# Optimization experiments

Hardware: AMD Instinct MI355X
Metric: run time of the kernel (lower is better)

Reference implementation:

```python
import jax, jax.numpy as jnp
import numpy as np

B, S, D = 4, 4096, 768  # batch, seq_len, n_units
NEG = -1000000000.0      # masked_fill value from the torch source


def setup_inputs() -> dict:
    key = jax.random.key(0)
    ks = jax.random.split(key, 12)
    scale = 1.0 / np.sqrt(D)
    inp = {
        "query": jax.random.normal(ks[0], (B, S, D), jnp.float32),
        "key_": jax.random.normal(ks[1], (B, S, D), jnp.float32),
        "value": jax.random.normal(ks[2], (B, S, D), jnp.float32),
        # nn.Linear weights are [out, in]; forward computes x @ W.T + b
        "Wq": jax.random.normal(ks[3], (D, D), jnp.float32) * scale,
        "bq": jnp.zeros((D,), jnp.float32),
        "Wk": jax.random.normal(ks[4], (D, D), jnp.float32) * scale,
        "bk": jnp.zeros((D,), jnp.float32),
        "Wv": jax.random.normal(ks[5], (D, D), jnp.float32) * scale,
        "bv": jnp.zeros((D,), jnp.float32),
        "Wo": jax.random.normal(ks[6], (D, D), jnp.float32) * scale,
        "bo": jnp.zeros((D,), jnp.float32),
        # broadcastable causal mask [1, S, S]; 0 -> masked
        "mask": jnp.tril(jnp.ones((S, S), jnp.int32))[None, :, :],
    }
    return inp


def reference(query, key_, value, Wq, bq, Wk, bk, Wv, bv, Wo, bo, mask):
    # QKV projections (torch Linear: x @ W.T + b)
    q = jnp.einsum("bsd,ed->bse", query, Wq) + bq
    k = jnp.einsum("bsd,ed->bse", key_, Wk) + bk
    v = jnp.einsum("bsd,ed->bse", value, Wv) + bv
    # scores: NOTE source scales by n_units**0.5 (full model dim, no head split)
    weights = jnp.einsum("bqd,bkd->bqk", q, k) / jnp.sqrt(jnp.float32(D))
    weights = jnp.where(mask == 0, jnp.float32(NEG), weights)
    weights = jax.nn.softmax(weights, axis=-1)
    # dropout is identity in eval/deterministic reference
    attended = jnp.einsum("bqk,bkd->bqd", weights, v)
    return jnp.einsum("bsd,ed->bse", attended, Wo) + bo
```

## Files before the change

kernel.cpp:

```cpp
#include <hip/hip_runtime.h>
#include <hip/hip_bf16.h>
#include <stdint.h>

#define DI __device__ __forceinline__

typedef __bf16 bf16x4 __attribute__((ext_vector_type(4)));
typedef __bf16 bf16x8 __attribute__((ext_vector_type(8)));
typedef float  f32x4  __attribute__((ext_vector_type(4)));

static constexpr int  BATCH = 4;
static constexpr int  SEQ   = 4096;
static constexpr int  DIM   = 768;
static constexpr long TOK   = (long)BATCH * SEQ;
static constexpr int  QT    = SEQ / 128;
static constexpr int  NTRI  = QT * (QT + 1) / 2;
static constexpr float SCALE = 0.0360843918243516150f;

__global__ void cvt3_kernel(const float* __restrict__ a, const float* __restrict__ b,
                            const float* __restrict__ c, __bf16* __restrict__ oa,
                            __bf16* __restrict__ ob, __bf16* __restrict__ oc, long n4){
  const float* in  = blockIdx.y == 0 ? a : blockIdx.y == 1 ? b : c;
  __bf16*      out = blockIdx.y == 0 ? oa : blockIdx.y == 1 ? ob : oc;
  long i = (long)blockIdx.x * blockDim.x + threadIdx.x;
  const long stride = (long)gridDim.x * blockDim.x;
  for(; i < n4; i += stride){
    float4 v = ((const float4*)in)[i];
    bf16x4 o = { (__bf16)v.x, (__bf16)v.y, (__bf16)v.z, (__bf16)v.w };
    ((bf16x4*)out)[i] = o;
  }
}
__global__ void cvt4_kernel(const float* __restrict__ a, const float* __restrict__ b,
                            const float* __restrict__ c, const float* __restrict__ d,
                            __bf16* __restrict__ oa, __bf16* __restrict__ ob,
                            __bf16* __restrict__ oc, __bf16* __restrict__ od, long n4){
  const float* in  = blockIdx.y == 0 ? a : blockIdx.y == 1 ? b : blockIdx.y == 2 ? c : d;
  __bf16*      out = blockIdx.y == 0 ? oa : blockIdx.y == 1 ? ob : blockIdx.y == 2 ? oc : od;
  long i = (long)blockIdx.x * blockDim.x + threadIdx.x;
  const long stride = (long)gridDim.x * blockDim.x;
  for(; i < n4; i += stride){
    float4 v = ((const float4*)in)[i];
    bf16x4 o = { (__bf16)v.x, (__bf16)v.y, (__bf16)v.z, (__bf16)v.w };
    ((bf16x4*)out)[i] = o;
  }
}

DI int swz_off(int r, int c){ return (r << 7) + ((c ^ (r & 7)) << 4); }

template<int R>
DI void stage(const __bf16* __restrict__ src, long ld, char* lds, int tid){
  const int w = tid >> 6, l = tid & 63;
  const int rsub = l >> 3;
  const int kc   = (l & 7) ^ rsub;
  const __bf16* g = src + (long)(w * 8 + rsub) * ld + kc * 8;
  char* d = lds + (w << 10);
  #pragma unroll
  for(int i = 0; i < R / 64; ++i){
    __builtin_amdgcn_global_load_lds(
        (const __attribute__((address_space(1))) void*)(g + (long)(i * 64) * ld),
        (__attribute__((address_space(3))) void*)(d + i * 8192), 16, 0, 0);
  }
}

DI bf16x8 frag_ld(const char* lds, int row, int c){
  return *(const bf16x8*)(lds + swz_off(row, c));
}

DI void mma_tile(const char* As, const char* Bs, int lane, int wr, int wc, f32x4 acc[4][4]){
  #pragma unroll
  for(int kk = 0; kk < 2; ++kk){
    const int c = kk * 4 + (lane >> 4);
    bf16x8 a[4], b[4];
    #pragma unroll
    for(int i = 0; i < 4; ++i) a[i] = frag_ld(As, wr + i * 16 + (lane & 15), c);
    #pragma unroll
    for(int j = 0; j < 4; ++j) b[j] = frag_ld(Bs, wc + j * 16 + (lane & 15), c);
    #pragma unroll
    for(int i = 0; i < 4; ++i)
      #pragma unroll
      for(int j = 0; j < 4; ++j)
        acc[i][j] = __builtin_amdgcn_mfma_f32_16x16x32_bf16(a[i], b[j], acc[i][j], 0, 0, 0);
  }
}

template<class FA, class FB>
DI void kloop2(FA fa, long lda, FB fb, long ldb, int nt, int tid,
               char* As, char* Bs, f32x4 acc[4][4]){
  const int lane = tid & 63, w = tid >> 6;
  const int wr = (w >> 2) * 64, wc = (w & 3) * 64;
  for(int t = 0; t < nt; ++t){
    stage<128>(fa(t), lda, As, tid);
    stage<256>(fb(t), ldb, Bs, tid);
    __syncthreads();
    mma_tile(As, Bs, lane, wr, wc, acc);
    __syncthreads();
  }
}

DI void issue_unit(const __bf16* __restrict__ src, long ld, char* slab, int tid){
  const int w = tid >> 6, lane = tid & 63;
  #pragma unroll
  for(int r = 0; r < 2; ++r){
    const int row = w * 16 + (lane >> 2) + r * 128;
    const int c   = (lane & 3) ^ ((row >> 1) & 3);
    const __bf16* g = src + (long)row * ld + c * 8;
    __builtin_amdgcn_global_load_lds(
        (const __attribute__((address_space(1))) void*)g,
        (__attribute__((address_space(3))) void*)(slab + w * 1024 + r * 8192), 16, 0, 0);
  }
}

template<int G>
DI void mma16(f32x4 (&acc)[8][4], const bf16x8 (&a)[4], const bf16x8 (&b)[4]){
  __builtin_amdgcn_s_setprio(1);
  #pragma unroll
  for(int i = 0; i < 4; ++i)
    #pragma unroll
    for(int j = 0; j < 4; ++j)
      acc[G * 4 + i][j] =
          __builtin_amdgcn_mfma_f32_16x16x32_bf16(a[i], b[j], acc[G * 4 + i][j], 0, 0, 0);
  __builtin_amdgcn_s_setprio(0);
}
template<int G>
DI void rdA(bf16x8 (&a)[4], const char* LA, int sbase, const int (&offA)[8]){
  #pragma unroll
  for(int i = 0; i < 4; ++i) a[i] = *(const bf16x8*)(LA + sbase + offA[G * 4 + i]);
}
DI void rdB(bf16x8 (&b)[4], const char* LB, int sbase, const int (&offB)[4]){
  #pragma unroll
  for(int j = 0; j < 4; ++j) b[j] = *(const bf16x8*)(LB + sbase + offB[j]);
}
#define VMW(N) asm volatile("s_waitcnt vmcnt(" #N ")" ::: "memory")

template<class FA, class FB>
DI void kloop8(FA fa, long lda, FB fb, long ldb, int nt, int tid,
               char* L, f32x4 (&acc)[8][4]){
  const int lane = tid & 63, w = tid >> 6;
  int offA[8], offB[4];
  #pragma unroll
  for(int i = 0; i < 8; ++i){
    const int r = (w >> 2) * 128 + i * 16 + (lane & 15);
    offA[i] = r * 64 + ((((lane >> 4)) ^ ((r >> 1) & 3)) << 4);
  }
  #pragma unroll
  for(int j = 0; j < 4; ++j){
    const int r = (w & 3) * 64 + j * 16 + (lane & 15);
    offB[j] = r * 64 + ((((lane >> 4)) ^ ((r >> 1) & 3)) << 4);
  }
  char* LA = L;
  char* LB = L + 65536;
  auto AS = [](int s, int k){ return s * 32768 + k * 16384; };
  issue_unit(fa(0),      lda, LA + AS(0, 0), tid);
  issue_unit(fb(0),      ldb, LB + AS(0, 0), tid);
  issue_unit(fa(0) + 32, lda, LA + AS(0, 1), tid);
  issue_unit(fb(0) + 32, ldb, LB + AS(0, 1), tid);
  issue_unit(fa(1),      lda, LA + AS(1, 0), tid);
  issue_unit(fb(1),      ldb, LB + AS(1, 0), tid);
  bf16x8 a[4], b[4];
  for(int t = 0; t < nt; t += 2){
    const bool more = (t + 2 < nt);
    VMW(8); __builtin_amdgcn_s_barrier();
    issue_unit(fa(t + 1) + 32, lda, LA + AS(1, 1), tid);
    rdB(b, LB, AS(0, 0), offB);
    rdA<0>(a, LA, AS(0, 0), offA);  mma16<0>(acc, a, b);
    issue_unit(fb(t + 1) + 32, ldb, LB + AS(1, 1), tid);
    rdA<1>(a, LA, AS(0, 0), offA);  mma16<1>(acc, a, b);
    VMW(8); __builtin_amdgcn_s_barrier();
    if(more) issue_unit(fa(t + 2), lda, LA + AS(0, 0), tid);
    rdB(b, LB, AS(0, 1), offB);
    rdA<0>(a, LA, AS(0, 1), offA);  mma16<0>(acc, a, b);
    if(more) issue_unit(fb(t + 2), ldb, LB + AS(0, 0), tid);
    rdA<1>(a, LA, AS(0, 1), offA);  mma16<1>(acc, a, b);
    if(more){ VMW(8); } else { VMW(4); }
    __builtin_amdgcn_s_barrier();
    if(more) issue_unit(fa(t + 2) + 32, lda, LA + AS(0, 1), tid);
    rdB(b, LB, AS(1, 0), offB);
    rdA<0>(a, LA, AS(1, 0), offA);  mma16<0>(acc, a, b);
    if(more) issue_unit(fb(t + 2) + 32, ldb, LB + AS(0, 1), tid);
    rdA<1>(a, LA, AS(1, 0), offA);  mma16<1>(acc, a, b);
    if(more){ VMW(8); } else { VMW(0); }
    __builtin_amdgcn_s_barrier();
    if(more) issue_unit(fa(t + 3), lda, LA + AS(1, 0), tid);
    rdB(b, LB, AS(1, 1), offB);
    rdA<0>(a, LA, AS(1, 1), offA);  mma16<0>(acc, a, b);
    if(more) issue_unit(fb(t + 3), ldb, LB + AS(1, 0), tid);
    rdA<1>(a, LA, AS(1, 1), offA);  mma16<1>(acc, a, b);
  }
}

DI int xcd_swz(int bid, int n){ const int c = n >> 3; return (bid & 7) * c + (bid >> 3); }

__global__ __launch_bounds__(512, 2)
void proj_qkv(const __bf16* __restrict__ xq, const __bf16* __restrict__ xk,
              const __bf16* __restrict__ xv, const __bf16* __restrict__ Wqb,
              const __bf16* __restrict__ Wkb, const __bf16* __restrict__ Wvb,
              const float* __restrict__ bq, const float* __restrict__ bk,
              const float* __restrict__ bv, __bf16* __restrict__ qb,
              __bf16* __restrict__ kb, __bf16* __restrict__ vbT){
  __shared__ __attribute__((aligned(128))) char L[131072];
  const int z = blockIdx.y, tid = threadIdx.x;
  const int bid = xcd_swz(blockIdx.x, 192);
  const __bf16 *A, *B; const float* bias; __bf16* C;
  long m0, n0, ldc; bool biasm;
  if(z == 0){ A = xq;  B = Wqb; bias = bq; C = qb;
              m0 = (long)(bid / 3) * 256; n0 = (bid % 3) * 256; ldc = DIM; biasm = false; }
  else if(z == 1){ A = xk;  B = Wkb; bias = bk; C = kb;
              m0 = (long)(bid / 3) * 256; n0 = (bid % 3) * 256; ldc = DIM; biasm = false; }
  else {      A = Wvb; B = xv;  bias = bv; C = vbT;
              m0 = (long)(bid / 64) * 256; n0 = (bid % 64) * 256; ldc = TOK; biasm = true; }
  const __bf16* Ar = A + m0 * DIM;
  const __bf16* Br = B + n0 * DIM;
  f32x4 acc[8][4] = {};
  auto fa = [&](int t){ return Ar + t * 64; };
  auto fb = [&](int t){ return Br + t * 64; };
  kloop8(fa, DIM, fb, DIM, DIM / 64, tid, L, acc);

  const int lane = tid & 63, w = tid >> 6;
  const int cl = lane & 15, rq = (lane >> 4) * 4;
  #pragma unroll
  for(int i = 0; i < 8; ++i)
    #pragma unroll
    for(int j = 0; j < 4; ++j){
      const long gc = n0 + (w & 3) * 64 + j * 16 + cl;
      #pragma unroll
      for(int e = 0; e < 4; ++e){
        const long gr = m0 + (w >> 2) * 128 + i * 16 + rq + e;
        C[gr * ldc + gc] = (__bf16)(acc[i][j][e] + bias[biasm ? gr : gc]);
      }
    }
}

__global__ __launch_bounds__(512, 2)
void qk_kernel(const __bf16* __restrict__ qb, const __bf16* __restrict__ kb,
               __bf16* __restrict__ Pc){
  __shared__ __attribute__((aligned(128))) char L[131072];
  const int b = blockIdx.y, tid = threadIdx.x;
  const int t = xcd_swz(blockIdx.x, 136);
  int Qi = (int)((sqrtf(8.0f * t + 1.0f) - 1.0f) * 0.5f);
  while((Qi + 1) * (Qi + 2) / 2 <= t) Qi++;
  while(Qi * (Qi + 1) / 2 > t) Qi--;
  const int Ki = t - Qi * (Qi + 1) / 2;
  const __bf16* Aq = qb + ((long)b * SEQ + Qi * 256) * DIM;
  const __bf16* Bk = kb + ((long)b * SEQ + Ki * 256) * DIM;
  f32x4 acc[8][4] = {};
  auto fa = [&](int t_){ return Aq + t_ * 64; };
  auto fb = [&](int t_){ return Bk + t_ * 64; };
  kloop8(fa, DIM, fb, DIM, DIM / 64, tid, L, acc);

  const int lane = tid & 63, w = tid >> 6;
  const int cl = lane & 15, rq = (lane >> 4) * 4;
  const int qi = 2 * Qi + (w >> 2);
  #pragma unroll
  for(int j = 0; j < 4; ++j){
    const int kw = (w & 3) * 64 + j * 16;
    const int ki = 2 * Ki + (kw >> 7);
    if(ki > qi) continue;
    const bool diag = (ki == qi);
    __bf16* tile = Pc + ((long)b * NTRI + (long)qi * (qi + 1) / 2 + ki) * 16384;
    const int kcol = (kw & 127) + cl;
    #pragma unroll
    for(int i = 0; i < 8; ++i){
      #pragma unroll
      for(int e = 0; e < 4; ++e){
        const int rloc = i * 16 + rq + e;
        float p = (diag && kcol > rloc) ? 0.0f
                  : __expf(fminf(acc[i][j][e] * SCALE, 30.0f));
        tile[rloc * 128 + kcol] = (__bf16)p;
      }
    }
  }
}

__global__ void rowsum(const __bf16* __restrict__ Pc, float* __restrict__ rlrow){
  const int gr = blockIdx.x * 4 + (threadIdx.x >> 6);
  const int lane = threadIdx.x & 63;
  const int b = gr >> 12, r = gr & 4095;
  const int qi = r >> 7, rloc = r & 127;
  const __bf16* base = Pc + ((long)b * NTRI + (long)qi * (qi + 1) / 2) * 16384
                       + rloc * 128;
  float s = 0.f;
  for(int ki = 0; ki <= qi; ++ki){
    uint32_t u = *(const uint32_t*)(base + (long)ki * 16384 + lane * 2);
    s += __uint_as_float(u << 16) + __uint_as_float(u & 0xffff0000u);
  }
  #pragma unroll
  for(int off = 32; off; off >>= 1) s += __shfl_xor(s, off);
  if(lane == 0) rlrow[gr] = 1.0f / s;
}

__global__ __launch_bounds__(512)
void pv_kernel(const __bf16* __restrict__ Pc, const float* __restrict__ rlrow,
               const __bf16* __restrict__ vbT, __bf16* __restrict__ att){
  __shared__ __attribute__((aligned(128))) char As[16384];
  __shared__ __attribute__((aligned(128))) char Bs[32768];
  __shared__ float sRl[128];
  const int b = blockIdx.z, qi = 31 - blockIdx.y, tid = threadIdx.x;
  const long n0 = (long)blockIdx.x * 256;
  if(tid < 128) sRl[tid] = rlrow[b * SEQ + qi * 128 + tid];
  const __bf16* Pq = Pc + ((long)b * NTRI + (long)qi * (qi + 1) / 2) * 16384;
  const __bf16* Bv = vbT + n0 * TOK + (long)b * SEQ;
  f32x4 acc[4][4] = {};
  auto fa = [&](int t){ return Pq + (long)(t >> 1) * 16384 + (t & 1) * 64; };
  auto fb = [&](int t){ return Bv + t * 64; };
  kloop2(fa, 128, fb, TOK, 2 * (qi + 1), tid, As, Bs, acc);

  const int lane = tid & 63, w = tid >> 6;
  const int wr = (w >> 2) * 64, wc = (w & 3) * 64;
  const int cl = lane & 15, rq = (lane >> 4) * 4;
  #pragma unroll
  for(int i = 0; i < 4; ++i)
    #pragma unroll
    for(int j = 0; j < 4; ++j){
      const long gc = n0 + wc + j * 16 + cl;
      #pragma unroll
      for(int e = 0; e < 4; ++e){
        const int rloc = wr + i * 16 + rq + e;
        float v = acc[i][j][e] * sRl[rloc];
        att[((long)b * SEQ + qi * 128 + rloc) * DIM + gc] = (__bf16)v;
      }
    }
}

__global__ __launch_bounds__(512)
void oproj(const __bf16* __restrict__ att, const __bf16* __restrict__ Wob,
           const float* __restrict__ bo, float* __restrict__ out){
  __shared__ __attribute__((aligned(128))) char As[16384];
  __shared__ __attribute__((aligned(128))) char Bs[32768];
  const int bid = blockIdx.x, tid = threadIdx.x;
  const long n0 = (bid % 3) * 256, m0 = (long)(bid / 3) * 128;
  const __bf16* Ar = att + m0 * DIM;
  const __bf16* Br = Wob + n0 * DIM;
  f32x4 acc[4][4] = {};
  auto fa = [&](int t){ return Ar + t * 64; };
  auto fb = [&](int t){ return Br + t * 64; };
  kloop2(fa, DIM, fb, DIM, DIM / 64, tid, As, Bs, acc);
  const int lane = tid & 63, w = tid >> 6;
  const int wr = (w >> 2) * 64, wc = (w & 3) * 64;
  const int cl = lane & 15, rq = (lane >> 4) * 4;
  #pragma unroll
  for(int i = 0; i < 4; ++i)
    #pragma unroll
    for(int j = 0; j < 4; ++j){
      const long gc = n0 + wc + j * 16 + cl;
      #pragma unroll
      for(int e = 0; e < 4; ++e){
        const long gr = m0 + wr + i * 16 + rq + e;
        out[gr * DIM + gc] = acc[i][j][e] + bo[gc];
      }
    }
}

extern "C" void kernel_launch(void* const* d_in, const int* in_sizes, int n_in,
                              void* d_out, int out_size, void* d_ws, size_t ws_size,
                              hipStream_t stream){
  const float* query = (const float*)d_in[0];
  const float* key_  = (const float*)d_in[1];
  const float* value = (const float*)d_in[2];
  const float* Wq = (const float*)d_in[3];
  const float* bq = (const float*)d_in[4];
  const float* Wk = (const float*)d_in[5];
  const float* bk = (const float*)d_in[6];
  const float* Wv = (const float*)d_in[7];
  const float* bv = (const float*)d_in[8];
  const float* Wo = (const float*)d_in[9];
  const float* bo = (const float*)d_in[10];

  char* p = (char*)d_ws;
  auto carve = [&](size_t bytes)->char*{
    char* r = p; p += (bytes + 255) & ~(size_t)255; return r;
  };
  const size_t tb = (size_t)TOK * DIM * 2;
  __bf16* xq  = (__bf16*)carve(tb);
  __bf16* xk  = (__bf16*)carve(tb);
  __bf16* xv  = (__bf16*)carve(tb);
  __bf16* qb  = (__bf16*)carve(tb);
  __bf16* kb  = (__bf16*)carve(tb);
  __bf16* vbT = (__bf16*)carve(tb);
  __bf16* Wqb = (__bf16*)carve((size_t)DIM * DIM * 2);
  __bf16* Wkb = (__bf16*)carve((size_t)DIM * DIM * 2);
  __bf16* Wvb = (__bf16*)carve((size_t)DIM * DIM * 2);
  __bf16* Wob = (__bf16*)carve((size_t)DIM * DIM * 2);
  __bf16* Pc  = (__bf16*)carve((size_t)BATCH * NTRI * 16384 * 2);
  float*  rlr = (float*)carve((size_t)TOK * 4);
  __bf16* att = xq;
  if((size_t)(p - (char*)d_ws) > ws_size) return;

  const long nIn4 = TOK * DIM / 4, nW4 = (long)DIM * DIM / 4;
  dim3 g3(2048, 3), g4((unsigned)((nW4 + 255) / 256), 4);
  cvt3_kernel<<<g3, 256, 0, stream>>>(query, key_, value, xq, xk, xv, nIn4);
  cvt4_kernel<<<g4, 256, 0, stream>>>(Wq, Wk, Wv, Wo, Wqb, Wkb, Wvb, Wob, nW4);

  proj_qkv<<<dim3(192, 3), 512, 0, stream>>>(xq, xk, xv, Wqb, Wkb, Wvb,
                                             bq, bk, bv, qb, kb, vbT);

  qk_kernel<<<dim3(136, BATCH), 512, 0, stream>>>(qb, kb, Pc);

  rowsum<<<TOK / 4, 256, 0, stream>>>(Pc, rlr);

  pv_kernel<<<dim3(3, QT, BATCH), 512, 0, stream>>>(Pc, rlr, vbT, att);

  oproj<<<384, 512, 0, stream>>>(att, Wob, bo, (float*)d_out);
}
```

Before: 339.8 us.

## Fuse row sums into QK kernel, split PV along keys, add halves in oproj

The QK kernel now works on smaller 256x128 tiles over a flat 1088-block grid and accumulates row sums with atomics, which removes the separate rowsum pass. The PV kernel splits each query block's key range into two halves written to separate buffers, giving more, better-balanced blocks. The output projection sums the two partial attention buffers while staging them into shared memory. In exchange it adds atomic traffic, a memset, and extra memory writes and reads for the second partial buffer.

After: 286.3 us (median of 2 runs). 15.7% less time.

```diff
diff --git a/kernel.cpp b/kernel.cpp
--- a/kernel.cpp
+++ b/kernel.cpp
@@ -46,18 +46,39 @@
 
 DI int swz_off(int r, int c){ return (r << 7) + ((c ^ (r & 7)) << 4); }
 
-template<int R>
+template<int NT, int R>
 DI void stage(const __bf16* __restrict__ src, long ld, char* lds, int tid){
   const int w = tid >> 6, l = tid & 63;
   const int rsub = l >> 3;
   const int kc   = (l & 7) ^ rsub;
   const __bf16* g = src + (long)(w * 8 + rsub) * ld + kc * 8;
   char* d = lds + (w << 10);
-  #pragma unroll
-  for(int i = 0; i < R / 64; ++i){
+  constexpr int RPC = NT / 8;
+  #pragma unroll
+  for(int i = 0; i < R / RPC; ++i){
     __builtin_amdgcn_global_load_lds(
-        (const __attribute__((address_space(1))) void*)(g + (long)(i * 64) * ld),
-        (__attribute__((address_space(3))) void*)(d + i * 8192), 16, 0, 0);
+        (const __attribute__((address_space(1))) void*)(g + (long)(i * RPC) * ld),
+        (__attribute__((address_space(3))) void*)(d + i * RPC * 128), 16, 0, 0);
+  }
+}
+
+template<int NT, int R>
+DI void stage_add(const __bf16* __restrict__ a0, const __bf16* __restrict__ a1,
+                  long ld, char* lds, int tid){
+  const int w = tid >> 6, l = tid & 63;
+  const int rsub = l >> 3;
+  const int kc   = (l & 7) ^ rsub;
+  const long off = (long)(w * 8 + rsub) * ld + kc * 8;
+  char* d = lds + (w << 10) + (l << 4);
+  constexpr int RPC = NT / 8;
+  #pragma unroll
+  for(int i = 0; i < R / RPC; ++i){
+    bf16x8 v0 = *(const bf16x8*)(a0 + off + (long)(i * RPC) * ld);
+    bf16x8 v1 = *(const bf16x8*)(a1 + off + (long)(i * RPC) * ld);
+    bf16x8 o;
+    #pragma unroll
+    for(int e = 0; e < 8; ++e) o[e] = (__bf16)((float)v0[e] + (float)v1[e]);
+    *(bf16x8*)(d + i * RPC * 128) = o;
   }
 }
 
@@ -88,8 +109,8 @@
   const int lane = tid & 63, w = tid >> 6;
   const int wr = (w >> 2) * 64, wc = (w & 3) * 64;
   for(int t = 0; t < nt; ++t){
-    stage<128>(fa(t), lda, As, tid);
-    stage<256>(fb(t), ldb, Bs, tid);
+    stage<512, 128>(fa(t), lda, As, tid);
+    stage<512, 256>(fb(t), ldb, Bs, tid);
     __syncthreads();
     mma_tile(As, Bs, lane, wr, wc, acc);
     __syncthreads();
@@ -229,80 +250,89 @@
     }
 }
 
-__global__ __launch_bounds__(512, 2)
+__global__ __launch_bounds__(512)
 void qk_kernel(const __bf16* __restrict__ qb, const __bf16* __restrict__ kb,
-               __bf16* __restrict__ Pc){
-  __shared__ __attribute__((aligned(128))) char L[131072];
-  const int b = blockIdx.y, tid = threadIdx.x;
-  const int t = xcd_swz(blockIdx.x, 136);
-  int Qi = (int)((sqrtf(8.0f * t + 1.0f) - 1.0f) * 0.5f);
-  while((Qi + 1) * (Qi + 2) / 2 <= t) Qi++;
-  while(Qi * (Qi + 1) / 2 > t) Qi--;
-  const int Ki = t - Qi * (Qi + 1) / 2;
+               __bf16* __restrict__ Pc, float* __restrict__ rlsum){
+  const int sid = xcd_swz(blockIdx.x, 1088);
+  const int b = sid / 272, t2 = sid % 272, tid = threadIdx.x;
+  int Qi = (int)((sqrtf(4.0f * t2 + 1.0f) - 1.0f) * 0.5f);
+  while((Qi + 1) * (Qi + 2) <= t2) Qi++;
+  while(Qi * (Qi + 1) > t2) Qi--;
+  const int ki = t2 - Qi * (Qi + 1);
   const __bf16* Aq = qb + ((long)b * SEQ + Qi * 256) * DIM;
-  const __bf16* Bk = kb + ((long)b * SEQ + Ki * 256) * DIM;
-  f32x4 acc[8][4] = {};
-  auto fa = [&](int t_){ return Aq + t_ * 64; };
-  auto fb = [&](int t_){ return Bk + t_ * 64; };
-  kloop8(fa, DIM, fb, DIM, DIM / 64, tid, L, acc);
-
-  const int lane = tid & 63, w = tid >> 6;
+  const __bf16* Bk = kb + ((long)b * SEQ + ki * 128) * DIM;
+  __shared__ __attribute__((aligned(128))) char As[32768];
+  __shared__ __attribute__((aligned(128))) char Bs[16384];
+  const int lane = tid & 63, w = tid >> 6;
+  const int wr = (w >> 1) * 64, wc = (w & 1) * 64;
+  f32x4 acc[4][4] = {};
+  for(int t = 0; t < DIM / 64; ++t){
+    stage<512, 256>(Aq + t * 64, DIM, As, tid);
+    stage<512, 128>(Bk + t * 64, DIM, Bs, tid);
+    __syncthreads();
+    mma_tile(As, Bs, lane, wr, wc, acc);
+    __syncthreads();
+  }
   const int cl = lane & 15, rq = (lane >> 4) * 4;
-  const int qi = 2 * Qi + (w >> 2);
-  #pragma unroll
-  for(int j = 0; j < 4; ++j){
-    const int kw = (w & 3) * 64 + j * 16;
-    const int ki = 2 * Ki + (kw >> 7);
+  #pragma unroll
+  for(int i = 0; i < 4; ++i){
+    const int rbase = wr + i * 16;
+    const int qi = 2 * Qi + (rbase >> 7);
     if(ki > qi) continue;
     const bool diag = (ki == qi);
     __bf16* tile = Pc + ((long)b * NTRI + (long)qi * (qi + 1) / 2 + ki) * 16384;
-    const int kcol = (kw & 127) + cl;
-    #pragma unroll
-    for(int i = 0; i < 8; ++i){
+    float rsum[4] = {0.f, 0.f, 0.f, 0.f};
+    #pragma unroll
+    for(int j = 0; j < 4; ++j){
+      const int c = wc + j * 16 + cl;
       #pragma unroll
       for(int e = 0; e < 4; ++e){
-        const int rloc = i * 16 + rq + e;
-        float p = (diag && kcol > rloc) ? 0.0f
+        const int rloc = (rbase + rq + e) & 127;
+        float p = (diag && c > rloc) ? 0.0f
                   : __expf(fminf(acc[i][j][e] * SCALE, 30.0f));
-        tile[rloc * 128 + kcol] = (__bf16)p;
+        tile[rloc * 128 + c] = (__bf16)p;
+        rsum[e] += p;
       }
     }
-  }
-}
-
-__global__ void rowsum(const __bf16* __restrict__ Pc, float* __restrict__ rlrow){
-  const int gr = blockIdx.x * 4 + (threadIdx.x >> 6);
-  const int lane = threadIdx.x & 63;
-  const int b = gr >> 12, r = gr & 4095;
-  const int qi = r >> 7, rloc = r & 127;
-  const __bf16* base = Pc + ((long)b * NTRI + (long)qi * (qi + 1) / 2) * 16384
-                       + rloc * 128;
-  float s = 0.f;
-  for(int ki = 0; ki <= qi; ++ki){
-    uint32_t u = *(const uint32_t*)(base + (long)ki * 16384 + lane * 2);
-    s += __uint_as_float(u << 16) + __uint_as_float(u & 0xffff0000u);
-  }
-  #pragma unroll
-  for(int off = 32; off; off >>= 1) s += __shfl_xor(s, off);
-  if(lane == 0) rlrow[gr] = 1.0f / s;
+    #pragma unroll
+    for(int e = 0; e < 4; ++e){
+      float s = rsum[e];
+      s += __shfl_xor(s, 1); s += __shfl_xor(s, 2);
+      s += __shfl_xor(s, 4); s += __shfl_xor(s, 8);
+      if(cl == 0){
+        const long gr = (long)b * SEQ + Qi * 256 + rbase + rq + e;
+        atomicAdd(&rlsum[gr], s);
+      }
+    }
+  }
 }
 
 __global__ __launch_bounds__(512)
-void pv_kernel(const __bf16* __restrict__ Pc, const float* __restrict__ rlrow,
-               const __bf16* __restrict__ vbT, __bf16* __restrict__ att){
+void pv_kernel(const __bf16* __restrict__ Pc, const float* __restrict__ rlsum,
+               const __bf16* __restrict__ vbT, __bf16* __restrict__ att0,
+               __bf16* __restrict__ att1){
   __shared__ __attribute__((aligned(128))) char As[16384];
   __shared__ __attribute__((aligned(128))) char Bs[32768];
   __shared__ float sRl[128];
-  const int b = blockIdx.z, qi = 31 - blockIdx.y, tid = threadIdx.x;
-  const long n0 = (long)blockIdx.x * 256;
-  if(tid < 128) sRl[tid] = rlrow[b * SEQ + qi * 128 + tid];
+  const int x = blockIdx.x, y = blockIdx.y, tid = threadIdx.x;
+  const long n0 = (long)(x >> 2) * 256;
+  const int b = x & 3;
+  int qi, k0, k1, half;
+  if(y == 62){ qi = 0; k0 = 0; k1 = 1; half = 0; }
+  else{
+    qi = 31 - (y >> 1); half = y & 1;
+    const int c0 = (qi + 2) >> 1;
+    if(half == 0){ k0 = 0; k1 = c0; } else { k0 = c0; k1 = qi + 1; }
+  }
+  if(tid < 128) sRl[tid] = 1.0f / rlsum[b * SEQ + qi * 128 + tid];
   const __bf16* Pq = Pc + ((long)b * NTRI + (long)qi * (qi + 1) / 2) * 16384;
   const __bf16* Bv = vbT + n0 * TOK + (long)b * SEQ;
   f32x4 acc[4][4] = {};
-  auto fa = [&](int t){ return Pq + (long)(t >> 1) * 16384 + (t & 1) * 64; };
-  auto fb = [&](int t){ return Bv + t * 64; };
-  kloop2(fa, 128, fb, TOK, 2 * (qi + 1), tid, As, Bs, acc);
-
+  auto fa = [&](int t){ return Pq + (long)(k0 + (t >> 1)) * 16384 + (t & 1) * 64; };
+  auto fb = [&](int t){ return Bv + (long)k0 * 128 + t * 64; };
+  kloop2(fa, 128, fb, TOK, 2 * (k1 - k0), tid, As, Bs, acc);
+
+  __bf16* dst = half ? att1 : att0;
   const int lane = tid & 63, w = tid >> 6;
   const int wr = (w >> 2) * 64, wc = (w & 3) * 64;
   const int cl = lane & 15, rq = (lane >> 4) * 4;
@@ -315,26 +345,38 @@
       for(int e = 0; e < 4; ++e){
         const int rloc = wr + i * 16 + rq + e;
         float v = acc[i][j][e] * sRl[rloc];
-        att[((long)b * SEQ + qi * 128 + rloc) * DIM + gc] = (__bf16)v;
+        dst[((long)b * SEQ + qi * 128 + rloc) * DIM + gc] = (__bf16)v;
       }
     }
+  if(y == 62){
+    const int r = tid >> 2;
+    const int c0 = (tid & 3) * 64;
+    __bf16* z0 = att1 + ((long)b * SEQ + r) * DIM + n0 + c0;
+    bf16x8 zz = {};
+    #pragma unroll
+    for(int i = 0; i < 8; ++i) *(bf16x8*)(z0 + i * 8) = zz;
+  }
 }
 
 __global__ __launch_bounds__(512)
-void oproj(const __bf16* __restrict__ att, const __bf16* __restrict__ Wob,
-           const float* __restrict__ bo, float* __restrict__ out){
+void oproj(const __bf16* __restrict__ att0, const __bf16* __restrict__ att1,
+           const __bf16* __restrict__ Wob, const float* __restrict__ bo,
+           float* __restrict__ out){
   __shared__ __attribute__((aligned(128))) char As[16384];
   __shared__ __attribute__((aligned(128))) char Bs[32768];
   const int bid = blockIdx.x, tid = threadIdx.x;
   const long n0 = (bid % 3) * 256, m0 = (long)(bid / 3) * 128;
-  const __bf16* Ar = att + m0 * DIM;
   const __bf16* Br = Wob + n0 * DIM;
   f32x4 acc[4][4] = {};
-  auto fa = [&](int t){ return Ar + t * 64; };
-  auto fb = [&](int t){ return Br + t * 64; };
-  kloop2(fa, DIM, fb, DIM, DIM / 64, tid, As, Bs, acc);
   const int lane = tid & 63, w = tid >> 6;
   const int wr = (w >> 2) * 64, wc = (w & 3) * 64;
+  for(int t = 0; t < DIM / 64; ++t){
+    stage_add<512, 128>(att0 + m0 * DIM + t * 64, att1 + m0 * DIM + t * 64, DIM, As, tid);
+    stage<512, 256>(Br + t * 64, DIM, Bs, tid);
+    __syncthreads();
+    mma_tile(As, Bs, lane, wr, wc, acc);
+    __syncthreads();
+  }
   const int cl = lane & 15, rq = (lane >> 4) * 4;
   #pragma unroll
   for(int i = 0; i < 4; ++i)
@@ -381,22 +423,22 @@
   __bf16* Wob = (__bf16*)carve((size_t)DIM * DIM * 2);
   __bf16* Pc  = (__bf16*)carve((size_t)BATCH * NTRI * 16384 * 2);
   float*  rlr = (float*)carve((size_t)TOK * 4);
-  __bf16* att = xq;
+  __bf16* att0 = xq;
+  __bf16* att1 = xk;
   if((size_t)(p - (char*)d_ws) > ws_size) return;
 
   const long nIn4 = TOK * DIM / 4, nW4 = (long)DIM * DIM / 4;
   dim3 g3(2048, 3), g4((unsigned)((nW4 + 255) / 256), 4);
+  hipMemsetAsync(rlr, 0, (size_t)TOK * 4, stream);
   cvt3_kernel<<<g3, 256, 0, stream>>>(query, key_, value, xq, xk, xv, nIn4);
   cvt4_kernel<<<g4, 256, 0, stream>>>(Wq, Wk, Wv, Wo, Wqb, Wkb, Wvb, Wob, nW4);
 
   proj_qkv<<<dim3(192, 3), 512, 0, stream>>>(xq, xk, xv, Wqb, Wkb, Wvb,
                                              bq, bk, bv, qb, kb, vbT);
 
-  qk_kernel<<<dim3(136, BATCH), 512, 0, stream>>>(qb, kb, Pc);
-
-  rowsum<<<TOK / 4, 256, 0, stream>>>(Pc, rlr);
-
-  pv_kernel<<<dim3(3, QT, BATCH), 512, 0, stream>>>(Pc, rlr, vbT, att);
-
-  oproj<<<384, 512, 0, stream>>>(att, Wob, bo, (float*)d_out);
-}
+  qk_kernel<<<1088, 512, 0, stream>>>(qb, kb, Pc, rlr);
+
+  pv_kernel<<<dim3(12, 63), 512, 0, stream>>>(Pc, rlr, vbT, att0, att1);
+
+  oproj<<<384, 512, 0, stream>>>(att0, att1, Wob, bo, (float*)d_out);
+}
```
